# Optimization experiments

Measured on AMD Instinct MI355X. Metric: run time of the kernel, lower is better.

## Reference

```python
import jax, jax.numpy as jnp
import numpy as np
import math

B, S, D, H = 2, 2048, 1024, 16
DK = D // H

def setup_inputs() -> dict:
    key = jax.random.key(0)
    ks = jax.random.split(key, 12)
    std = 1.0 / math.sqrt(D)
    inp = {
        'query': jax.random.normal(ks[0], (B, S, D), jnp.float32),
        'key':   jax.random.normal(ks[1], (B, S, D), jnp.float32),
        'value': jax.random.normal(ks[2], (B, S, D), jnp.float32),
        'mask':  jnp.ones((B, 1, 1, S), dtype=bool),
        'wq': jax.random.normal(ks[3], (D, D), jnp.float32) * std,
        'bq': jnp.zeros((D,), jnp.float32),
        'wk': jax.random.normal(ks[4], (D, D), jnp.float32) * std,
        'bk': jnp.zeros((D,), jnp.float32),
        'wv': jax.random.normal(ks[5], (D, D), jnp.float32) * std,
        'bv': jnp.zeros((D,), jnp.float32),
        'wo': jax.random.normal(ks[6], (D, D), jnp.float32) * std,
        'bo': jnp.zeros((D,), jnp.float32),
    }
    return inp

def reference(query, key, value, mask, wq, bq, wk, bk, wv, bv, wo, bo):
    # torch.nn.Linear: y = x @ W^T + b
    def split_heads(x):  # [B,S,D] -> [B,H,S,DK]
        return x.reshape(B, -1, H, DK).transpose(0, 2, 1, 3)
    Q = split_heads(query @ wq.T + bq)
    K = split_heads(key @ wk.T + bk)
    V = split_heads(value @ wv.T + bv)
    scale = 1.0 / math.sqrt(DK)
    scores = jnp.einsum('bhtd,bhsd->bhts', Q, K * scale)  # [B,H,S,S]
    scores = jnp.where(mask, scores, -jnp.inf)
    attn = jax.nn.softmax(scores, axis=-1)
    # dropout p=0.0 (eval) -> identity
    context = jnp.einsum('bhts,bhsd->bhtd', attn, V)
    context = context.transpose(0, 2, 1, 3).reshape(B, -1, D)
    return context @ wo.T + bo
```

## Files before the change

kernel.cpp:

```cpp
#include <hip/hip_runtime.h>
#include <stdint.h>

#define SEQ 2048
#define NH  16

typedef __bf16 bf16x8 __attribute__((ext_vector_type(8)));
typedef float  f32x4  __attribute__((ext_vector_type(4)));

#if __has_builtin(__builtin_amdgcn_exp2f)
#define EXP2(x) __builtin_amdgcn_exp2f(x)
#else
#define EXP2(x) exp2f(x)
#endif

#define WAITV0 asm volatile("s_waitcnt vmcnt(0)" ::: "memory")
#define WAITV2 asm volatile("s_waitcnt vmcnt(2)" ::: "memory")
#define SBAR() do { __builtin_amdgcn_sched_barrier(0); __builtin_amdgcn_s_barrier(); __builtin_amdgcn_sched_barrier(0); } while (0)

__device__ __forceinline__ unsigned short f2bf(float f) {
  union { float f; uint32_t u; } v; v.f = f;
  uint32_t r = v.u + 0x7fffu + ((v.u >> 16) & 1u);
  return (unsigned short)(r >> 16);
}

__device__ __forceinline__ void gll16(const void* g, void* l) {
  __builtin_amdgcn_global_load_lds((const __attribute__((address_space(1))) void*)g,
                                   (__attribute__((address_space(3))) void*)l, 16, 0, 0);
}

__device__ __forceinline__ f32x4 mfma16(bf16x8 a, bf16x8 b, f32x4 c) {
  return __builtin_amdgcn_mfma_f32_16x16x32_bf16(a, b, c, 0, 0, 0);
}

struct CvtJobs {
  const float* s[7];
  unsigned short* d[7];
  int n4[7];
};

__global__ void cvt_all(CvtJobs J) {
  int j = blockIdx.y;
  const float* __restrict__ s = J.s[j];
  unsigned short* __restrict__ d = J.d[j];
  int n4 = J.n4[j];
  int st = gridDim.x * blockDim.x;
  for (int i = blockIdx.x * blockDim.x + threadIdx.x; i < n4; i += st) {
    float4 v = ((const float4*)s)[i];
    union { unsigned short u[4]; uint2 q; } o;
    o.u[0] = f2bf(v.x); o.u[1] = f2bf(v.y); o.u[2] = f2bf(v.z); o.u[3] = f2bf(v.w);
    ((uint2*)d)[i] = o.q;
  }
}

struct GemmJobs {
  const unsigned short* A[3];
  const unsigned short* W[3];
  const float* bias[3];
  void* out[3];
  float scale[3];
  int mode[3];
};

template<int BM, int NB>
__global__ __launch_bounds__(256, (BM == 128 ? 3 : 2)) void gemm_t(GemmJobs J) {
  __shared__ alignas(16) unsigned short Asm[BM * 64];
  __shared__ alignas(16) unsigned short Bsm[128 * 64];
  constexpr int MFR = BM / 32;
  constexpr int MB = 4096 / BM;
  const int tid = threadIdx.x;
  const int l = tid & 63, w = tid >> 6;
  const int wr = w >> 1, wc = w & 1;
  const int lg = l >> 4, lo = l & 15;

  const int nwg = gridDim.x;
  const int id = blockIdx.x;
  const int swz = (id & 7) * (nwg >> 3) + (id >> 3);
  const int g = swz / NB;
  const int rem = swz % NB;
  const int m0 = (rem % MB) * BM;
  const int n0 = (rem / MB) * 128;

  const unsigned short* __restrict__ A = J.A[g];
  const unsigned short* __restrict__ W = J.W[g];
  const float* __restrict__ bias = J.bias[g];
  const int mode = J.mode[g];
  const float scale = J.scale[g];

  f32x4 acc[MFR][4] = {};

  for (int kt = 0; kt < 16; ++kt) {
#pragma unroll
    for (int it = 0; it < BM / 32; ++it) {
      int chunk = it * 256 + tid;
      int row = chunk >> 3, c = chunk & 7;
      const char* src = (const char*)A + (((size_t)(m0 + row) << 10) + (kt << 6)) * 2 + ((c ^ (row & 7)) << 4);
      gll16(src, (char*)Asm + ((it * 256 + (tid & ~63)) << 4));
    }
#pragma unroll
    for (int it = 0; it < 4; ++it) {
      int chunk = it * 256 + tid;
      int row = chunk >> 3, c = chunk & 7;
      const char* src = (const char*)W + (((size_t)(n0 + row) << 10) + (kt << 6)) * 2 + ((c ^ (row & 7)) << 4);
      gll16(src, (char*)Bsm + ((it * 256 + (tid & ~63)) << 4));
    }
    WAITV0;
    SBAR();
#pragma unroll
    for (int kf = 0; kf < 2; ++kf) {
      bf16x8 af[MFR], bfr[4];
#pragma unroll
      for (int mf = 0; mf < MFR; ++mf) {
        int row = wr * (BM / 2) + mf * 16 + lo;
        int pos = (kf * 4 + lg) ^ (row & 7);
        af[mf] = *(const bf16x8*)((const char*)Asm + row * 128 + pos * 16);
      }
#pragma unroll
      for (int nf = 0; nf < 4; ++nf) {
        int row = wc * 64 + nf * 16 + lo;
        int pos = (kf * 4 + lg) ^ (row & 7);
        bfr[nf] = *(const bf16x8*)((const char*)Bsm + row * 128 + pos * 16);
      }
#pragma unroll
      for (int mf = 0; mf < MFR; ++mf)
#pragma unroll
        for (int nf = 0; nf < 4; ++nf)
          acc[mf][nf] = mfma16(af[mf], bfr[nf], acc[mf][nf]);
    }
    SBAR();
  }

#pragma unroll
  for (int mf = 0; mf < MFR; ++mf)
#pragma unroll
    for (int nf = 0; nf < 4; ++nf) {
      int gcol = n0 + wc * 64 + nf * 16 + lo;
      float bv = bias[gcol];
#pragma unroll
      for (int r = 0; r < 4; ++r) {
        int grow = m0 + wr * (BM / 2) + mf * 16 + lg * 4 + r;
        float v = (acc[mf][nf][r] + bv) * scale;
        if (mode == 2) {
          ((float*)J.out[g])[((size_t)grow << 10) + gcol] = v;
        } else {
          int b = grow >> 11, s = grow & 2047, h = gcol >> 6, dk = gcol & 63;
          size_t idx;
          if (mode == 0) idx = ((((size_t)((b << 4) + h) << 11) + s) << 6) + dk;
          else           idx = ((((size_t)((b << 4) + h) << 6) + dk) << 11) + s;
          ((__bf16*)J.out[g])[idx] = (__bf16)v;
        }
      }
    }
}

__global__ __launch_bounds__(512, 2) void attn_kernel(const unsigned short* __restrict__ Qb,
                                                      const unsigned short* __restrict__ Kb,
                                                      const unsigned short* __restrict__ Vt,
                                                      unsigned short* __restrict__ ctx) {
  __shared__ alignas(16) unsigned short Ksm[2][64 * 64];
  __shared__ alignas(16) unsigned short Vsm[2][64 * 64];
  __shared__ alignas(16) unsigned short Psm[8 * 16 * 64];
  const int tid = threadIdx.x;
  const int l = tid & 63, w = tid >> 6;
  const int lg = l >> 4, lo = l & 15;
  const int sw = lo & 7;

  const int id = blockIdx.x;
  const int swz = (id & 7) * 64 + (id >> 3);
  const int bh = swz >> 4;
  const int qt = swz & 15;

  const unsigned short* Qp = Qb + (size_t)bh * SEQ * 64;
  const unsigned short* Kp = Kb + (size_t)bh * SEQ * 64;
  const unsigned short* Vp = Vt + (size_t)bh * 64 * SEQ;
  const int q0 = qt * 128 + w * 16;

  bf16x8 qf[2];
#pragma unroll
  for (int kc = 0; kc < 2; ++kc)
    qf[kc] = *(const bf16x8*)((const char*)Qp + (((size_t)(q0 + lo)) << 7) + kc * 64 + lg * 16);
  WAITV0;

  f32x4 O[4] = {};
  float m_ = -1e30f, l_ = 0.f;

#define ASTAGE(b, t)                                                                      \
  do {                                                                                    \
    const int kv0s = (t) << 6;                                                            \
    int row = tid >> 3, c = tid & 7;                                                      \
    const char* ksrc = (const char*)Kp + ((size_t)(kv0s + row) << 7) + ((c ^ (row & 7)) << 4); \
    gll16(ksrc, (char*)Ksm[b] + ((tid & ~63) << 4));                                      \
    const char* vsrc = (const char*)Vp + ((size_t)row << 12) + (kv0s << 1) + ((c ^ (row & 7)) << 4); \
    gll16(vsrc, (char*)Vsm[b] + ((tid & ~63) << 4));                                      \
  } while (0)

  ASTAGE(0, 0);

  for (int t = 0; t < SEQ / 64; ++t) {
    const int cur = t & 1;
    if (t < SEQ / 64 - 1) {
      ASTAGE(cur ^ 1, t + 1);
      WAITV2;
    } else {
      WAITV0;
    }
    SBAR();

    f32x4 sfr[4] = {};
#pragma unroll
    for (int kc = 0; kc < 2; ++kc) {
      bf16x8 kfr[4];
#pragma unroll
      for (int kvf = 0; kvf < 4; ++kvf) {
        int kv = kvf * 16 + lo;
        int pos = (kc * 4 + lg) ^ (kv & 7);
        kfr[kvf] = *(const bf16x8*)((const char*)Ksm[cur] + kv * 128 + pos * 16);
      }
#pragma unroll
      for (int kvf = 0; kvf < 4; ++kvf)
        sfr[kvf] = mfma16(kfr[kvf], qf[kc], sfr[kvf]);
    }

    float a0 = fmaxf(fmaxf(sfr[0][0], sfr[0][1]), fmaxf(sfr[0][2], sfr[0][3]));
    float a1 = fmaxf(fmaxf(sfr[1][0], sfr[1][1]), fmaxf(sfr[1][2], sfr[1][3]));
    float a2 = fmaxf(fmaxf(sfr[2][0], sfr[2][1]), fmaxf(sfr[2][2], sfr[2][3]));
    float a3 = fmaxf(fmaxf(sfr[3][0], sfr[3][1]), fmaxf(sfr[3][2], sfr[3][3]));
    float mx = fmaxf(fmaxf(a0, a1), fmaxf(a2, a3));
    mx = fmaxf(mx, __shfl_xor(mx, 16));
    mx = fmaxf(mx, __shfl_xor(mx, 32));

    if (__any((int)(mx > m_))) {
      float mnew = fmaxf(m_, mx);
      float fac = EXP2(m_ - mnew);
      m_ = mnew;
      float ps = 0.f;
#pragma unroll
      for (int kvf = 0; kvf < 4; ++kvf)
#pragma unroll
        for (int r = 0; r < 4; ++r) {
          float p = EXP2(sfr[kvf][r] - mnew);
          sfr[kvf][r] = p;
          ps += p;
        }
      ps += __shfl_xor(ps, 16);
      ps += __shfl_xor(ps, 32);
      l_ = l_ * fac + ps;
#pragma unroll
      for (int r = 0; r < 4; ++r) {
        float fb = __shfl(fac, lg * 4 + r);
#pragma unroll
        for (int dkf = 0; dkf < 4; ++dkf) O[dkf][r] *= fb;
      }
    } else {
      float ps = 0.f;
#pragma unroll
      for (int kvf = 0; kvf < 4; ++kvf)
#pragma unroll
        for (int r = 0; r < 4; ++r) {
          float p = EXP2(sfr[kvf][r] - m_);
          sfr[kvf][r] = p;
          ps += p;
        }
      ps += __shfl_xor(ps, 16);
      ps += __shfl_xor(ps, 32);
      l_ += ps;
    }

#pragma unroll
    for (int kvf = 0; kvf < 4; ++kvf) {
      union { __bf16 b[4]; unsigned long long u; } pk;
#pragma unroll
      for (int r = 0; r < 4; ++r) pk.b[r] = (__bf16)sfr[kvf][r];
      int g = kvf * 2 + (lg >> 1);
      *(unsigned long long*)((char*)Psm + w * 2048 + lo * 128 + ((g ^ sw) << 4) + ((lg & 1) << 3)) = pk.u;
    }

    bf16x8 af[2];
#pragma unroll
    for (int kc = 0; kc < 2; ++kc) {
      int pos = (kc * 4 + lg) ^ sw;
      af[kc] = *(const bf16x8*)((const char*)Psm + w * 2048 + lo * 128 + pos * 16);
    }
#pragma unroll
    for (int dkf = 0; dkf < 4; ++dkf) {
      int dk = dkf * 16 + lo;
      int pos0 = lg ^ (dk & 7);
      int pos1 = (4 + lg) ^ (dk & 7);
      bf16x8 bv0 = *(const bf16x8*)((const char*)Vsm[cur] + dk * 128 + pos0 * 16);
      bf16x8 bv1 = *(const bf16x8*)((const char*)Vsm[cur] + dk * 128 + pos1 * 16);
      O[dkf] = mfma16(af[0], bv0, O[dkf]);
      O[dkf] = mfma16(af[1], bv1, O[dkf]);
    }
    SBAR();
  }
#undef ASTAGE

  const int b = bh >> 4, h = bh & 15;
#pragma unroll
  for (int r = 0; r < 4; ++r) {
    float lr = __shfl(l_, lg * 4 + r);
    float inv = 1.f / lr;
    int srow = q0 + lg * 4 + r;
    size_t rowoff = ((size_t)(b * SEQ + srow) << 10) + h * 64;
#pragma unroll
    for (int dkf = 0; dkf < 4; ++dkf)
      ((__bf16*)ctx)[rowoff + dkf * 16 + lo] = (__bf16)(O[dkf][r] * inv);
  }
}

extern "C" void kernel_launch(void* const* d_in, const int* in_sizes, int n_in,
                              void* d_out, int out_size, void* d_ws, size_t ws_size,
                              hipStream_t stream) {
  const float* query = (const float*)d_in[0];
  const float* key_  = (const float*)d_in[1];
  const float* value = (const float*)d_in[2];
  const float* wq = (const float*)d_in[4];
  const float* bq = (const float*)d_in[5];
  const float* wk = (const float*)d_in[6];
  const float* bk = (const float*)d_in[7];
  const float* wv = (const float*)d_in[8];
  const float* bv = (const float*)d_in[9];
  const float* wo = (const float*)d_in[10];
  const float* bo = (const float*)d_in[11];

  char* ws = (char*)d_ws;
  unsigned short* xq  = (unsigned short*)(ws + 0);
  unsigned short* xk  = (unsigned short*)(ws + 8388608);
  unsigned short* xv  = (unsigned short*)(ws + 16777216);
  unsigned short* wqb = (unsigned short*)(ws + 25165824);
  unsigned short* wkb = (unsigned short*)(ws + 27262976);
  unsigned short* wvb = (unsigned short*)(ws + 29360128);
  unsigned short* wob = (unsigned short*)(ws + 31457280);
  unsigned short* Qb  = (unsigned short*)(ws + 33554432);
  unsigned short* Kb  = (unsigned short*)(ws + 41943040);
  unsigned short* Vb  = (unsigned short*)(ws + 50331648);
  unsigned short* ctx = (unsigned short*)(ws + 58720256);

  CvtJobs cj;
  cj.s[0] = query; cj.d[0] = xq;  cj.n4[0] = 1048576;
  cj.s[1] = key_;  cj.d[1] = xk;  cj.n4[1] = 1048576;
  cj.s[2] = value; cj.d[2] = xv;  cj.n4[2] = 1048576;
  cj.s[3] = wq;    cj.d[3] = wqb; cj.n4[3] = 262144;
  cj.s[4] = wk;    cj.d[4] = wkb; cj.n4[4] = 262144;
  cj.s[5] = wv;    cj.d[5] = wvb; cj.n4[5] = 262144;
  cj.s[6] = wo;    cj.d[6] = wob; cj.n4[6] = 262144;
  cvt_all<<<dim3(256, 7), 256, 0, stream>>>(cj);

  const float kscale = 0.125f * 1.44269504088896340736f;
  GemmJobs gj;
  gj.A[0] = xq; gj.W[0] = wqb; gj.bias[0] = bq; gj.out[0] = (void*)Qb; gj.scale[0] = 1.0f;   gj.mode[0] = 0;
  gj.A[1] = xk; gj.W[1] = wkb; gj.bias[1] = bk; gj.out[1] = (void*)Kb; gj.scale[1] = kscale; gj.mode[1] = 0;
  gj.A[2] = xv; gj.W[2] = wvb; gj.bias[2] = bv; gj.out[2] = (void*)Vb; gj.scale[2] = 1.0f;   gj.mode[2] = 1;
  gemm_t<128, 256><<<768, 256, 0, stream>>>(gj);

  attn_kernel<<<512, 512, 0, stream>>>(Qb, Kb, Vb, ctx);

  GemmJobs oj;
  oj.A[0] = ctx; oj.W[0] = wob; oj.bias[0] = bo; oj.out[0] = d_out; oj.scale[0] = 1.0f; oj.mode[0] = 2;
  oj.A[1] = oj.A[0]; oj.W[1] = oj.W[0]; oj.bias[1] = oj.bias[0]; oj.out[1] = oj.out[0]; oj.scale[1] = 1.0f; oj.mode[1] = 2;
  oj.A[2] = oj.A[0]; oj.W[2] = oj.W[0]; oj.bias[2] = oj.bias[0]; oj.out[2] = oj.out[0]; oj.scale[2] = 1.0f; oj.mode[2] = 2;
  gemm_t<64, 512><<<512, 256, 0, stream>>>(oj);
}
```

Measured before the change: 148.5 us.

## Fuse fp32-to-bf16 conversion into GEMM loads and rework attention with 32x32 MFMA

Drops the separate conversion kernel. The GEMMs now read fp32 activations and weights directly and convert them to bf16 in registers before storing to LDS, which removes a full extra pass over the inputs and the bf16 staging buffers. The attention kernel moves to 4 waves of 32 query rows using 32x32x16 MFMA. P stays in registers through packed bf16 conversion and permlane32_swap instead of an LDS round trip, and s_setprio hints are added around the MFMA phases. In exchange, the GEMM loads become synchronous register loads rather than async global-to-LDS, and the weights are reconverted by every block that reads them.

```diff
diff --git a/kernel.cpp b/kernel.cpp
--- a/kernel.cpp
+++ b/kernel.cpp
@@ -6,6 +6,8 @@
 
 typedef __bf16 bf16x8 __attribute__((ext_vector_type(8)));
 typedef float  f32x4  __attribute__((ext_vector_type(4)));
+typedef float  f32x16 __attribute__((ext_vector_type(16)));
+typedef unsigned uint2v __attribute__((ext_vector_type(2)));
 
 #if __has_builtin(__builtin_amdgcn_exp2f)
 #define EXP2(x) __builtin_amdgcn_exp2f(x)
@@ -14,14 +16,8 @@
 #endif
 
 #define WAITV0 asm volatile("s_waitcnt vmcnt(0)" ::: "memory")
-#define WAITV2 asm volatile("s_waitcnt vmcnt(2)" ::: "memory")
+#define WAITV4 asm volatile("s_waitcnt vmcnt(4)" ::: "memory")
 #define SBAR() do { __builtin_amdgcn_sched_barrier(0); __builtin_amdgcn_s_barrier(); __builtin_amdgcn_sched_barrier(0); } while (0)
-
-__device__ __forceinline__ unsigned short f2bf(float f) {
-  union { float f; uint32_t u; } v; v.f = f;
-  uint32_t r = v.u + 0x7fffu + ((v.u >> 16) & 1u);
-  return (unsigned short)(r >> 16);
-}
 
 __device__ __forceinline__ void gll16(const void* g, void* l) {
   __builtin_amdgcn_global_load_lds((const __attribute__((address_space(1))) void*)g,
@@ -31,37 +27,20 @@
 __device__ __forceinline__ f32x4 mfma16(bf16x8 a, bf16x8 b, f32x4 c) {
   return __builtin_amdgcn_mfma_f32_16x16x32_bf16(a, b, c, 0, 0, 0);
 }
-
-struct CvtJobs {
-  const float* s[7];
-  unsigned short* d[7];
-  int n4[7];
-};
-
-__global__ void cvt_all(CvtJobs J) {
-  int j = blockIdx.y;
-  const float* __restrict__ s = J.s[j];
-  unsigned short* __restrict__ d = J.d[j];
-  int n4 = J.n4[j];
-  int st = gridDim.x * blockDim.x;
-  for (int i = blockIdx.x * blockDim.x + threadIdx.x; i < n4; i += st) {
-    float4 v = ((const float4*)s)[i];
-    union { unsigned short u[4]; uint2 q; } o;
-    o.u[0] = f2bf(v.x); o.u[1] = f2bf(v.y); o.u[2] = f2bf(v.z); o.u[3] = f2bf(v.w);
-    ((uint2*)d)[i] = o.q;
-  }
+__device__ __forceinline__ f32x16 mfma32(bf16x8 a, bf16x8 b, f32x16 c) {
+  return __builtin_amdgcn_mfma_f32_32x32x16_bf16(a, b, c, 0, 0, 0);
 }
 
 struct GemmJobs {
-  const unsigned short* A[3];
-  const unsigned short* W[3];
+  const void* A[3];
+  const float* W[3];
   const float* bias[3];
   void* out[3];
   float scale[3];
   int mode[3];
 };
 
-template<int BM, int NB>
+template<int BM, int NB, bool AFP32>
 __global__ __launch_bounds__(256, (BM == 128 ? 3 : 2)) void gemm_t(GemmJobs J) {
   __shared__ alignas(16) unsigned short Asm[BM * 64];
   __shared__ alignas(16) unsigned short Bsm[128 * 64];
@@ -80,8 +59,7 @@
   const int m0 = (rem % MB) * BM;
   const int n0 = (rem / MB) * 128;
 
-  const unsigned short* __restrict__ A = J.A[g];
-  const unsigned short* __restrict__ W = J.W[g];
+  const float* __restrict__ W = J.W[g];
   const float* __restrict__ bias = J.bias[g];
   const int mode = J.mode[g];
   const float scale = J.scale[g];
@@ -89,22 +67,44 @@
   f32x4 acc[MFR][4] = {};
 
   for (int kt = 0; kt < 16; ++kt) {
-#pragma unroll
-    for (int it = 0; it < BM / 32; ++it) {
-      int chunk = it * 256 + tid;
-      int row = chunk >> 3, c = chunk & 7;
-      const char* src = (const char*)A + (((size_t)(m0 + row) << 10) + (kt << 6)) * 2 + ((c ^ (row & 7)) << 4);
-      gll16(src, (char*)Asm + ((it * 256 + (tid & ~63)) << 4));
+    if constexpr (AFP32) {
+      const float* __restrict__ A = (const float*)J.A[g];
+#pragma unroll
+      for (int it = 0; it < BM / 32; ++it) {
+        int g8 = it * 256 + tid;
+        int row = g8 >> 3, c = g8 & 7;
+        const float* src = A + (((size_t)(m0 + row)) << 10) + (kt << 6) + c * 8;
+        float4 u0 = ((const float4*)src)[0];
+        float4 u1 = ((const float4*)src)[1];
+        union { __bf16 b[8]; bf16x8 v; } cv;
+        cv.b[0] = (__bf16)u0.x; cv.b[1] = (__bf16)u0.y; cv.b[2] = (__bf16)u0.z; cv.b[3] = (__bf16)u0.w;
+        cv.b[4] = (__bf16)u1.x; cv.b[5] = (__bf16)u1.y; cv.b[6] = (__bf16)u1.z; cv.b[7] = (__bf16)u1.w;
+        *(bf16x8*)((char*)Asm + row * 128 + ((c ^ (row & 7)) << 4)) = cv.v;
+      }
+    } else {
+      const unsigned short* __restrict__ A = (const unsigned short*)J.A[g];
+#pragma unroll
+      for (int it = 0; it < BM / 32; ++it) {
+        int chunk = it * 256 + tid;
+        int row = chunk >> 3, c = chunk & 7;
+        const char* src = (const char*)A + (((size_t)(m0 + row) << 10) + (kt << 6)) * 2 + ((c ^ (row & 7)) << 4);
+        gll16(src, (char*)Asm + ((it * 256 + (tid & ~63)) << 4));
+      }
     }
 #pragma unroll
     for (int it = 0; it < 4; ++it) {
-      int chunk = it * 256 + tid;
-      int row = chunk >> 3, c = chunk & 7;
-      const char* src = (const char*)W + (((size_t)(n0 + row) << 10) + (kt << 6)) * 2 + ((c ^ (row & 7)) << 4);
-      gll16(src, (char*)Bsm + ((it * 256 + (tid & ~63)) << 4));
-    }
-    WAITV0;
-    SBAR();
+      int g8 = it * 256 + tid;
+      int row = g8 >> 3, c = g8 & 7;
+      const float* src = W + (((size_t)(n0 + row)) << 10) + (kt << 6) + c * 8;
+      float4 u0 = ((const float4*)src)[0];
+      float4 u1 = ((const float4*)src)[1];
+      union { __bf16 b[8]; bf16x8 v; } cv;
+      cv.b[0] = (__bf16)u0.x; cv.b[1] = (__bf16)u0.y; cv.b[2] = (__bf16)u0.z; cv.b[3] = (__bf16)u0.w;
+      cv.b[4] = (__bf16)u1.x; cv.b[5] = (__bf16)u1.y; cv.b[6] = (__bf16)u1.z; cv.b[7] = (__bf16)u1.w;
+      *(bf16x8*)((char*)Bsm + row * 128 + ((c ^ (row & 7)) << 4)) = cv.v;
+    }
+    if constexpr (!AFP32) { WAITV0; }
+    __syncthreads();
 #pragma unroll
     for (int kf = 0; kf < 2; ++kf) {
       bf16x8 af[MFR], bfr[4];
@@ -126,7 +126,7 @@
         for (int nf = 0; nf < 4; ++nf)
           acc[mf][nf] = mfma16(af[mf], bfr[nf], acc[mf][nf]);
     }
-    SBAR();
+    __syncthreads();
   }
 
 #pragma unroll
@@ -152,17 +152,15 @@
     }
 }
 
-__global__ __launch_bounds__(512, 2) void attn_kernel(const unsigned short* __restrict__ Qb,
+__global__ __launch_bounds__(256, 2) void attn_kernel(const unsigned short* __restrict__ Qb,
                                                       const unsigned short* __restrict__ Kb,
                                                       const unsigned short* __restrict__ Vt,
                                                       unsigned short* __restrict__ ctx) {
   __shared__ alignas(16) unsigned short Ksm[2][64 * 64];
   __shared__ alignas(16) unsigned short Vsm[2][64 * 64];
-  __shared__ alignas(16) unsigned short Psm[8 * 16 * 64];
   const int tid = threadIdx.x;
   const int l = tid & 63, w = tid >> 6;
-  const int lg = l >> 4, lo = l & 15;
-  const int sw = lo & 7;
+  const int ql = l & 31, hi = l >> 5;
 
   const int id = blockIdx.x;
   const int swz = (id & 7) * 64 + (id >> 3);
@@ -172,25 +170,29 @@
   const unsigned short* Qp = Qb + (size_t)bh * SEQ * 64;
   const unsigned short* Kp = Kb + (size_t)bh * SEQ * 64;
   const unsigned short* Vp = Vt + (size_t)bh * 64 * SEQ;
-  const int q0 = qt * 128 + w * 16;
-
-  bf16x8 qf[2];
-#pragma unroll
-  for (int kc = 0; kc < 2; ++kc)
-    qf[kc] = *(const bf16x8*)((const char*)Qp + (((size_t)(q0 + lo)) << 7) + kc * 64 + lg * 16);
+  const int q0 = qt * 128 + w * 32;
+
+  bf16x8 qb[4];
+#pragma unroll
+  for (int c = 0; c < 4; ++c)
+    qb[c] = *(const bf16x8*)((const char*)Qp + (((size_t)(q0 + ql)) << 7) + c * 32 + hi * 16);
   WAITV0;
 
-  f32x4 O[4] = {};
+  f32x16 o0 = {}, o1 = {};
   float m_ = -1e30f, l_ = 0.f;
 
 #define ASTAGE(b, t)                                                                      \
   do {                                                                                    \
     const int kv0s = (t) << 6;                                                            \
-    int row = tid >> 3, c = tid & 7;                                                      \
-    const char* ksrc = (const char*)Kp + ((size_t)(kv0s + row) << 7) + ((c ^ (row & 7)) << 4); \
-    gll16(ksrc, (char*)Ksm[b] + ((tid & ~63) << 4));                                      \
-    const char* vsrc = (const char*)Vp + ((size_t)row << 12) + (kv0s << 1) + ((c ^ (row & 7)) << 4); \
-    gll16(vsrc, (char*)Vsm[b] + ((tid & ~63) << 4));                                      \
+    _Pragma("unroll")                                                                     \
+    for (int it = 0; it < 2; ++it) {                                                      \
+      int chunk = it * 256 + tid;                                                         \
+      int row = chunk >> 3, c = chunk & 7;                                                \
+      const char* ksrc = (const char*)Kp + ((size_t)(kv0s + row) << 7) + ((c ^ (row & 7)) << 4); \
+      gll16(ksrc, (char*)Ksm[b] + ((it * 256 + (tid & ~63)) << 4));                       \
+      const char* vsrc = (const char*)Vp + ((size_t)row << 12) + (kv0s << 1) + ((c ^ (row & 7)) << 4); \
+      gll16(vsrc, (char*)Vsm[b] + ((it * 256 + (tid & ~63)) << 4));                       \
+    }                                                                                     \
   } while (0)
 
   ASTAGE(0, 0);
@@ -199,111 +201,101 @@
     const int cur = t & 1;
     if (t < SEQ / 64 - 1) {
       ASTAGE(cur ^ 1, t + 1);
-      WAITV2;
+      WAITV4;
     } else {
       WAITV0;
     }
     SBAR();
 
-    f32x4 sfr[4] = {};
-#pragma unroll
-    for (int kc = 0; kc < 2; ++kc) {
-      bf16x8 kfr[4];
-#pragma unroll
-      for (int kvf = 0; kvf < 4; ++kvf) {
-        int kv = kvf * 16 + lo;
-        int pos = (kc * 4 + lg) ^ (kv & 7);
-        kfr[kvf] = *(const bf16x8*)((const char*)Ksm[cur] + kv * 128 + pos * 16);
-      }
-#pragma unroll
-      for (int kvf = 0; kvf < 4; ++kvf)
-        sfr[kvf] = mfma16(kfr[kvf], qf[kc], sfr[kvf]);
-    }
-
-    float a0 = fmaxf(fmaxf(sfr[0][0], sfr[0][1]), fmaxf(sfr[0][2], sfr[0][3]));
-    float a1 = fmaxf(fmaxf(sfr[1][0], sfr[1][1]), fmaxf(sfr[1][2], sfr[1][3]));
-    float a2 = fmaxf(fmaxf(sfr[2][0], sfr[2][1]), fmaxf(sfr[2][2], sfr[2][3]));
-    float a3 = fmaxf(fmaxf(sfr[3][0], sfr[3][1]), fmaxf(sfr[3][2], sfr[3][3]));
-    float mx = fmaxf(fmaxf(a0, a1), fmaxf(a2, a3));
-    mx = fmaxf(mx, __shfl_xor(mx, 16));
+    f32x16 s0 = {}, s1 = {};
+    __builtin_amdgcn_s_setprio(1);
+#pragma unroll
+    for (int c = 0; c < 4; ++c) {
+      int pr = c * 2 + hi;
+      bf16x8 k0 = *(const bf16x8*)((const char*)Ksm[cur] + ql * 128 + ((pr ^ (ql & 7)) << 4));
+      bf16x8 k1 = *(const bf16x8*)((const char*)Ksm[cur] + (32 + ql) * 128 + ((pr ^ ((32 + ql) & 7)) << 4));
+      s0 = mfma32(k0, qb[c], s0);
+      s1 = mfma32(k1, qb[c], s1);
+    }
+    __builtin_amdgcn_s_setprio(0);
+
+#define MAX4(v, i) fmaxf(fmaxf(v[i], v[i+1]), fmaxf(v[i+2], v[i+3]))
+    float mA = fmaxf(fmaxf(MAX4(s0, 0), MAX4(s0, 4)), fmaxf(MAX4(s0, 8), MAX4(s0, 12)));
+    float mB = fmaxf(fmaxf(MAX4(s1, 0), MAX4(s1, 4)), fmaxf(MAX4(s1, 8), MAX4(s1, 12)));
+    float mx = fmaxf(mA, mB);
     mx = fmaxf(mx, __shfl_xor(mx, 32));
+#undef MAX4
 
     if (__any((int)(mx > m_))) {
       float mnew = fmaxf(m_, mx);
       float fac = EXP2(m_ - mnew);
       m_ = mnew;
-      float ps = 0.f;
-#pragma unroll
-      for (int kvf = 0; kvf < 4; ++kvf)
-#pragma unroll
-        for (int r = 0; r < 4; ++r) {
-          float p = EXP2(sfr[kvf][r] - mnew);
-          sfr[kvf][r] = p;
-          ps += p;
-        }
-      ps += __shfl_xor(ps, 16);
+#pragma unroll
+      for (int r = 0; r < 16; ++r) { s0[r] = EXP2(s0[r] - mnew); s1[r] = EXP2(s1[r] - mnew); }
+#define SUM4(v, i) ((v[i] + v[i+1]) + (v[i+2] + v[i+3]))
+      float ps = ((SUM4(s0, 0) + SUM4(s0, 4)) + (SUM4(s0, 8) + SUM4(s0, 12)))
+               + ((SUM4(s1, 0) + SUM4(s1, 4)) + (SUM4(s1, 8) + SUM4(s1, 12)));
       ps += __shfl_xor(ps, 32);
       l_ = l_ * fac + ps;
 #pragma unroll
-      for (int r = 0; r < 4; ++r) {
-        float fb = __shfl(fac, lg * 4 + r);
-#pragma unroll
-        for (int dkf = 0; dkf < 4; ++dkf) O[dkf][r] *= fb;
+      for (int reg = 0; reg < 16; ++reg) {
+        int qrow = (reg & 3) + 8 * (reg >> 2) + 4 * hi;
+        float fb = __shfl(fac, qrow);
+        o0[reg] *= fb; o1[reg] *= fb;
       }
     } else {
-      float ps = 0.f;
-#pragma unroll
-      for (int kvf = 0; kvf < 4; ++kvf)
-#pragma unroll
-        for (int r = 0; r < 4; ++r) {
-          float p = EXP2(sfr[kvf][r] - m_);
-          sfr[kvf][r] = p;
-          ps += p;
-        }
-      ps += __shfl_xor(ps, 16);
+#pragma unroll
+      for (int r = 0; r < 16; ++r) { s0[r] = EXP2(s0[r] - m_); s1[r] = EXP2(s1[r] - m_); }
+      float ps = ((SUM4(s0, 0) + SUM4(s0, 4)) + (SUM4(s0, 8) + SUM4(s0, 12)))
+               + ((SUM4(s1, 0) + SUM4(s1, 4)) + (SUM4(s1, 8) + SUM4(s1, 12)));
       ps += __shfl_xor(ps, 32);
       l_ += ps;
-    }
-
-#pragma unroll
-    for (int kvf = 0; kvf < 4; ++kvf) {
-      union { __bf16 b[4]; unsigned long long u; } pk;
-#pragma unroll
-      for (int r = 0; r < 4; ++r) pk.b[r] = (__bf16)sfr[kvf][r];
-      int g = kvf * 2 + (lg >> 1);
-      *(unsigned long long*)((char*)Psm + w * 2048 + lo * 128 + ((g ^ sw) << 4) + ((lg & 1) << 3)) = pk.u;
-    }
-
-    bf16x8 af[2];
-#pragma unroll
-    for (int kc = 0; kc < 2; ++kc) {
-      int pos = (kc * 4 + lg) ^ sw;
-      af[kc] = *(const bf16x8*)((const char*)Psm + w * 2048 + lo * 128 + pos * 16);
-    }
-#pragma unroll
-    for (int dkf = 0; dkf < 4; ++dkf) {
-      int dk = dkf * 16 + lo;
-      int pos0 = lg ^ (dk & 7);
-      int pos1 = (4 + lg) ^ (dk & 7);
-      bf16x8 bv0 = *(const bf16x8*)((const char*)Vsm[cur] + dk * 128 + pos0 * 16);
-      bf16x8 bv1 = *(const bf16x8*)((const char*)Vsm[cur] + dk * 128 + pos1 * 16);
-      O[dkf] = mfma16(af[0], bv0, O[dkf]);
-      O[dkf] = mfma16(af[1], bv1, O[dkf]);
-    }
+#undef SUM4
+    }
+
+    bf16x8 pa[4];
+#pragma unroll
+    for (int c = 0; c < 4; ++c) {
+      const int rb = (c & 1) * 8;
+      float e0, e1, e2, e3, e4, e5, e6, e7;
+      if ((c >> 1) == 0) { e0=s0[rb]; e1=s0[rb+1]; e2=s0[rb+2]; e3=s0[rb+3]; e4=s0[rb+4]; e5=s0[rb+5]; e6=s0[rb+6]; e7=s0[rb+7]; }
+      else               { e0=s1[rb]; e1=s1[rb+1]; e2=s1[rb+2]; e3=s1[rb+3]; e4=s1[rb+4]; e5=s1[rb+5]; e6=s1[rb+6]; e7=s1[rb+7]; }
+      unsigned X0, X1, Z0, Z1;
+      asm("v_cvt_pk_bf16_f32 %0, %1, %2" : "=v"(X0) : "v"(e0), "v"(e1));
+      asm("v_cvt_pk_bf16_f32 %0, %1, %2" : "=v"(X1) : "v"(e2), "v"(e3));
+      asm("v_cvt_pk_bf16_f32 %0, %1, %2" : "=v"(Z0) : "v"(e4), "v"(e5));
+      asm("v_cvt_pk_bf16_f32 %0, %1, %2" : "=v"(Z1) : "v"(e6), "v"(e7));
+      uint2v rA = __builtin_amdgcn_permlane32_swap(X0, Z0, false, false);
+      uint2v rB = __builtin_amdgcn_permlane32_swap(X1, Z1, false, false);
+      union { unsigned u[4]; bf16x8 v; } pk_;
+      pk_.u[0] = rA[0]; pk_.u[1] = rB[0]; pk_.u[2] = rA[1]; pk_.u[3] = rB[1];
+      pa[c] = pk_.v;
+    }
+
+    __builtin_amdgcn_s_setprio(1);
+#pragma unroll
+    for (int c = 0; c < 4; ++c) {
+      int pr = c * 2 + hi;
+      bf16x8 v0 = *(const bf16x8*)((const char*)Vsm[cur] + ql * 128 + ((pr ^ (ql & 7)) << 4));
+      bf16x8 v1 = *(const bf16x8*)((const char*)Vsm[cur] + (32 + ql) * 128 + ((pr ^ ((32 + ql) & 7)) << 4));
+      o0 = mfma32(pa[c], v0, o0);
+      o1 = mfma32(pa[c], v1, o1);
+    }
+    __builtin_amdgcn_s_setprio(0);
     SBAR();
   }
 #undef ASTAGE
 
   const int b = bh >> 4, h = bh & 15;
 #pragma unroll
-  for (int r = 0; r < 4; ++r) {
-    float lr = __shfl(l_, lg * 4 + r);
+  for (int reg = 0; reg < 16; ++reg) {
+    int qrow = (reg & 3) + 8 * (reg >> 2) + 4 * hi;
+    float lr = __shfl(l_, qrow);
     float inv = 1.f / lr;
-    int srow = q0 + lg * 4 + r;
-    size_t rowoff = ((size_t)(b * SEQ + srow) << 10) + h * 64;
-#pragma unroll
-    for (int dkf = 0; dkf < 4; ++dkf)
-      ((__bf16*)ctx)[rowoff + dkf * 16 + lo] = (__bf16)(O[dkf][r] * inv);
+    int srow = q0 + qrow;
+    size_t off = (((size_t)(b * SEQ + srow)) << 10) + h * 64 + ql;
+    ((__bf16*)ctx)[off]      = (__bf16)(o0[reg] * inv);
+    ((__bf16*)ctx)[off + 32] = (__bf16)(o1[reg] * inv);
   }
 }
 
@@ -323,40 +315,23 @@
   const float* bo = (const float*)d_in[11];
 
   char* ws = (char*)d_ws;
-  unsigned short* xq  = (unsigned short*)(ws + 0);
-  unsigned short* xk  = (unsigned short*)(ws + 8388608);
-  unsigned short* xv  = (unsigned short*)(ws + 16777216);
-  unsigned short* wqb = (unsigned short*)(ws + 25165824);
-  unsigned short* wkb = (unsigned short*)(ws + 27262976);
-  unsigned short* wvb = (unsigned short*)(ws + 29360128);
-  unsigned short* wob = (unsigned short*)(ws + 31457280);
-  unsigned short* Qb  = (unsigned short*)(ws + 33554432);
-  unsigned short* Kb  = (unsigned short*)(ws + 41943040);
-  unsigned short* Vb  = (unsigned short*)(ws + 50331648);
-  unsigned short* ctx = (unsigned short*)(ws + 58720256);
-
-  CvtJobs cj;
-  cj.s[0] = query; cj.d[0] = xq;  cj.n4[0] = 1048576;
-  cj.s[1] = key_;  cj.d[1] = xk;  cj.n4[1] = 1048576;
-  cj.s[2] = value; cj.d[2] = xv;  cj.n4[2] = 1048576;
-  cj.s[3] = wq;    cj.d[3] = wqb; cj.n4[3] = 262144;
-  cj.s[4] = wk;    cj.d[4] = wkb; cj.n4[4] = 262144;
-  cj.s[5] = wv;    cj.d[5] = wvb; cj.n4[5] = 262144;
-  cj.s[6] = wo;    cj.d[6] = wob; cj.n4[6] = 262144;
-  cvt_all<<<dim3(256, 7), 256, 0, stream>>>(cj);
+  unsigned short* Qb  = (unsigned short*)(ws + 0);
+  unsigned short* Kb  = (unsigned short*)(ws + 8388608);
+  unsigned short* Vb  = (unsigned short*)(ws + 16777216);
+  unsigned short* ctx = (unsigned short*)(ws + 25165824);
 
   const float kscale = 0.125f * 1.44269504088896340736f;
   GemmJobs gj;
-  gj.A[0] = xq; gj.W[0] = wqb; gj.bias[0] = bq; gj.out[0] = (void*)Qb; gj.scale[0] = 1.0f;   gj.mode[0] = 0;
-  gj.A[1] = xk; gj.W[1] = wkb; gj.bias[1] = bk; gj.out[1] = (void*)Kb; gj.scale[1] = kscale; gj.mode[1] = 0;
-  gj.A[2] = xv; gj.W[2] = wvb; gj.bias[2] = bv; gj.out[2] = (void*)Vb; gj.scale[2] = 1.0f;   gj.mode[2] = 1;
-  gemm_t<128, 256><<<768, 256, 0, stream>>>(gj);
-
-  attn_kernel<<<512, 512, 0, stream>>>(Qb, Kb, Vb, ctx);
+  gj.A[0] = query; gj.W[0] = wq; gj.bias[0] = bq; gj.out[0] = (void*)Qb; gj.scale[0] = 1.0f;   gj.mode[0] = 0;
+  gj.A[1] = key_;  gj.W[1] = wk; gj.bias[1] = bk; gj.out[1] = (void*)Kb; gj.scale[1] = kscale; gj.mode[1] = 0;
+  gj.A[2] = value; gj.W[2] = wv; gj.bias[2] = bv; gj.out[2] = (void*)Vb; gj.scale[2] = 1.0f;   gj.mode[2] = 1;
+  gemm_t<128, 256, true><<<768, 256, 0, stream>>>(gj);
+
+  attn_kernel<<<512, 256, 0, stream>>>(Qb, Kb, Vb, ctx);
 
   GemmJobs oj;
-  oj.A[0] = ctx; oj.W[0] = wob; oj.bias[0] = bo; oj.out[0] = d_out; oj.scale[0] = 1.0f; oj.mode[0] = 2;
+  oj.A[0] = ctx; oj.W[0] = wo; oj.bias[0] = bo; oj.out[0] = d_out; oj.scale[0] = 1.0f; oj.mode[0] = 2;
   oj.A[1] = oj.A[0]; oj.W[1] = oj.W[0]; oj.bias[1] = oj.bias[0]; oj.out[1] = oj.out[0]; oj.scale[1] = 1.0f; oj.mode[1] = 2;
   oj.A[2] = oj.A[0]; oj.W[2] = oj.W[0]; oj.bias[2] = oj.bias[0]; oj.out[2] = oj.out[0]; oj.scale[2] = 1.0f; oj.mode[2] = 2;
-  gemm_t<64, 512><<<512, 256, 0, stream>>>(oj);
-}
+  gemm_t<64, 512, false><<<512, 256, 0, stream>>>(oj);
+}
```

Result: slower. 181.6 us (+22.3%).
